# Optimization experiments

Hardware: AMD Instinct MI355X
Metric: run time of the kernel (lower is better)

The kernel has to match this reference:

```python
import jax, jax.numpy as jnp
import numpy as np

N = 100000      # nodes
E = 1200000     # edges (avg degree ~12)
D_IN = 64
D_OUT = 64


def setup_inputs() -> dict:
    key = jax.random.key(0)
    k1, k2, k3, k4 = jax.random.split(key, 4)
    x = jax.random.normal(k1, (N, D_IN), dtype=jnp.float32)
    # learned params (glorot-ish init)
    W = jax.random.normal(k2, (D_IN, D_OUT), dtype=jnp.float32) / np.sqrt(D_IN).astype(np.float32)
    b = jnp.zeros((D_OUT,), dtype=jnp.float32)
    src = jax.random.randint(k3, (E,), 0, N, dtype=jnp.int32)
    dst = jax.random.randint(k4, (E,), 0, N, dtype=jnp.int32)
    return {"x": x, "W": W, "b": b, "src": src, "dst": dst}


def reference(x, W, b, src, dst):
    # GCN layer: h = relu( D^-1/2 A D^-1/2 (x @ W) + b ), dropout=0 (eval)
    ones = jnp.ones(src.shape[0], dtype=x.dtype)
    deg_out = jax.ops.segment_sum(ones, src, num_segments=N)   # out-degree of source nodes
    deg_in = jax.ops.segment_sum(ones, dst, num_segments=N)    # in-degree of dest nodes
    norm_src = jax.lax.rsqrt(jnp.maximum(deg_out, 1.0))
    norm_dst = jax.lax.rsqrt(jnp.maximum(deg_in, 1.0))

    h = x @ W                                                  # [N, D_OUT] dense transform
    msg = h[src] * norm_src[src][:, None]                      # [E, D_OUT] gathered, pre-normalized messages
    agg = jax.ops.segment_sum(msg, dst, num_segments=N)        # [N, D_OUT] sparse aggregation
    out = agg * norm_dst[:, None] + b
    return jax.nn.relu(out)
```

## Files before the change

kernel.cpp:

```cpp
#include <hip/hip_runtime.h>
#include <hip/hip_bf16.h>

#define N_NODES 100000
#define N_EDGES 1200000
#define DCH 64

#define FB 256
#define NT 1024
#define EPB 4688
#define PPB 2344
#define HPAIRS 4688
#define GW_TOT (FB * NT / 64)

#define HALF_BINS 50000
#define HALF_WORDS 12500

#define BNODES 128
#define KBUK ((N_NODES + BNODES - 1) / BNODES)
#define CAPE 3008

#define NT2 512

#define OFF_DEG      0
#define OFF_GCUR     100096
#define OFF_FLAG     103296
#define OFF_ESORT    103424
#define OFF_HS       9512704

__device__ __forceinline__ float load_f(const void* p, int i, int f32) {
    if (f32) return ((const float*)p)[i];
    return __bfloat162float(((const __hip_bfloat16*)p)[i]);
}

__device__ __forceinline__ unsigned short f2bf_bits(float f) {
    __hip_bfloat16 h = __float2bfloat16(f);
    return __builtin_bit_cast(unsigned short, h);
}

__global__ __launch_bounds__(NT, 4)
void fused_kernel(const int* __restrict__ src,
                  const int* __restrict__ dst,
                  const void* __restrict__ x,
                  const void* __restrict__ W,
                  unsigned int* __restrict__ deg_packed,
                  int* __restrict__ gcur,
                  unsigned int* __restrict__ esort,
                  int* __restrict__ flag,
                  __hip_bfloat16* __restrict__ hs) {
    __shared__ unsigned int h[HALF_WORDS];
    int tid = threadIdx.x;
    int bid = blockIdx.x;

    int* sn = (int*)h;
    if (tid == 0) sn[0] = 0;
    __syncthreads();
    if (tid < 256) {
        const unsigned short* u = (const unsigned short*)x;
        int c = 0;
        for (int i = tid * 16; i < tid * 16 + 16; ++i) {
            unsigned short v = u[2 * i];
            int e = (v >> 7) & 0xFF;
            if (e >= 141) c++;
        }
        if (c) atomicAdd(sn, c);
    }
    __syncthreads();
    int f32 = sn[0] > 256;
    if (bid == 0 && tid == 0) *flag = f32;
    __syncthreads();

    {
        float* wt = (float*)h;
        for (int i = tid; i < DCH * DCH; i += NT) {
            int kk = i >> 6, cc = i & 63;
            wt[cc * 68 + kk] = load_f(W, i, f32);
        }
        __syncthreads();

        int lane = tid & 63;
        const float4* wrow = (const float4*)(wt + lane * 68);
        float wr[DCH];
#pragma unroll
        for (int kq = 0; kq < 16; ++kq) {
            float4 t = wrow[kq];
            wr[4 * kq + 0] = t.x; wr[4 * kq + 1] = t.y;
            wr[4 * kq + 2] = t.z; wr[4 * kq + 3] = t.w;
        }
#pragma unroll
        for (int kk = 0; kk < DCH; ++kk)
            asm volatile("" : "+v"(wr[kk]));

        int gw = (bid << 4) + (tid >> 6);
#define RLA(i) __int_as_float(__builtin_amdgcn_readlane(xiA, (i)))
#define RLB(i) __int_as_float(__builtin_amdgcn_readlane(xiB, (i)))
#define GRP(j) \
    a0 = fmaf(RLA(4*(j)+0), wr[4*(j)+0], a0); \
    a1 = fmaf(RLA(4*(j)+1), wr[4*(j)+1], a1); \
    a2 = fmaf(RLA(4*(j)+2), wr[4*(j)+2], a2); \
    a3 = fmaf(RLA(4*(j)+3), wr[4*(j)+3], a3); \
    c0 = fmaf(RLB(4*(j)+0), wr[4*(j)+0], c0); \
    c1 = fmaf(RLB(4*(j)+1), wr[4*(j)+1], c1); \
    c2 = fmaf(RLB(4*(j)+2), wr[4*(j)+2], c2); \
    c3 = fmaf(RLB(4*(j)+3), wr[4*(j)+3], c3);

        for (int node = gw; node < N_NODES; node += 2 * GW_TOT) {
            int nodeB = node + GW_TOT;
            int hasB = nodeB < N_NODES;
            float xvA = load_f(x, node * DCH + lane, f32);
            float xvB = hasB ? load_f(x, nodeB * DCH + lane, f32) : 0.0f;
            int xiA = __float_as_int(xvA);
            int xiB = __float_as_int(xvB);
            float a0 = 0.f, a1 = 0.f, a2 = 0.f, a3 = 0.f;
            float c0 = 0.f, c1 = 0.f, c2 = 0.f, c3 = 0.f;
            GRP(0)  GRP(1)  GRP(2)  GRP(3)
            GRP(4)  GRP(5)  GRP(6)  GRP(7)
            GRP(8)  GRP(9)  GRP(10) GRP(11)
            GRP(12) GRP(13) GRP(14) GRP(15)
            hs[node * DCH + lane] = __float2bfloat16((a0 + a1) + (a2 + a3));
            if (hasB)
                hs[nodeB * DCH + lane] = __float2bfloat16((c0 + c1) + (c2 + c3));
        }
#undef RLA
#undef RLB
#undef GRP
    }
    __syncthreads();

    {
        int half = bid & 1;
        int j = bid >> 1;
        int p0 = j * HPAIRS;
        int p1 = p0 + HPAIRS;
        if (p1 > N_EDGES / 2) p1 = N_EDGES / 2;
        const int2* s2 = (const int2*)src;
        for (int w = tid; w < HALF_WORDS; w += NT) h[w] = 0;
        __syncthreads();
        int lo = half * HALF_BINS;
        for (int p = p0 + tid; p < p1; p += NT) {
            int2 sp = s2[p];
            int n0 = sp.x - lo, n1 = sp.y - lo;
            if ((unsigned)n0 < (unsigned)HALF_BINS)
                atomicAdd(&h[n0 >> 2], 1u << ((n0 & 3) * 8));
            if ((unsigned)n1 < (unsigned)HALF_BINS)
                atomicAdd(&h[n1 >> 2], 1u << ((n1 & 3) * 8));
        }
        __syncthreads();
        unsigned int* dp = deg_packed + half * HALF_WORDS;
        for (int w = tid; w < HALF_WORDS; w += NT) {
            unsigned int v = h[w];
            if (v) atomicAdd(&dp[w], v);
        }
        __syncthreads();
    }

    {
        int e0 = bid * EPB;
        int eend = e0 + EPB; if (eend > N_EDGES) eend = N_EDGES;
        int npair = (eend - e0) >> 1;
        const int2* src2 = (const int2*)(src + e0);
        const int2* dst2 = (const int2*)(dst + e0);

        int* cnt  = (int*)h;
        int* base = cnt + KBUK;
        int* cur  = base + KBUK;
        for (int i = tid; i < KBUK; i += NT) { cnt[i] = 0; cur[i] = 0; }
        __syncthreads();
        for (int p = tid; p < npair; p += NT) {
            int2 dp = dst2[p];
            atomicAdd(&cnt[dp.x >> 7], 1);
            atomicAdd(&cnt[dp.y >> 7], 1);
        }
        __syncthreads();
        for (int i = tid; i < KBUK; i += NT)
            base[i] = atomicAdd(&gcur[i], cnt[i]);
        __syncthreads();
        for (int p = tid; p < npair; p += NT) {
            int2 sp = src2[p];
            int2 dp = dst2[p];
            int b0 = dp.x >> 7, b1 = dp.y >> 7;
            int pos0 = base[b0] + atomicAdd(&cur[b0], 1);
            if (pos0 < CAPE)
                esort[b0 * CAPE + pos0] =
                    (unsigned int)sp.x | ((unsigned int)(dp.x & 127) << 24);
            int pos1 = base[b1] + atomicAdd(&cur[b1], 1);
            if (pos1 < CAPE)
                esort[b1 * CAPE + pos1] =
                    (unsigned int)sp.y | ((unsigned int)(dp.y & 127) << 24);
        }
    }
}

__global__ __launch_bounds__(NT2, 6)
void sortgather_kernel(const __hip_bfloat16* __restrict__ hs,
                       const unsigned int* __restrict__ esort,
                       const int* __restrict__ gcur,
                       const unsigned int* __restrict__ deg_packed,
                       const void* __restrict__ b,
                       const int* __restrict__ flag,
                       void* __restrict__ out) {
    __shared__ unsigned int ebuf[CAPE];
    __shared__ int cnt[BNODES];
    __shared__ int loc[BNODES];
    __shared__ int sc[BNODES];
    __shared__ int cur[BNODES];
    __shared__ float tab[256];
    int k = blockIdx.x, tid = threadIdx.x;
    int bbase = k * CAPE;
    int m = gcur[k];
    if (m > CAPE) m = CAPE;

    if (tid < BNODES) { cnt[tid] = 0; cur[tid] = 0; }
    if (tid < 256) tab[tid] = rsqrtf(fmaxf((float)tid, 1.0f));
    __syncthreads();
    for (int e = tid; e < m; e += NT2)
        atomicAdd(&cnt[esort[bbase + e] >> 24], 1);
    __syncthreads();
    int v = 0;
    if (tid < BNODES) { v = cnt[tid]; sc[tid] = v; }
    __syncthreads();
    for (int off = 1; off < BNODES; off <<= 1) {
        int add = 0;
        if (tid < BNODES && tid >= off) add = sc[tid - off];
        __syncthreads();
        if (tid < BNODES) sc[tid] += add;
        __syncthreads();
    }
    if (tid < BNODES) loc[tid] = sc[tid] - v;
    __syncthreads();
    for (int e = tid; e < m; e += NT2) {
        unsigned int w = esort[bbase + e];
        int r = w >> 24;
        unsigned int s = w & 0xFFFFFFu;
        unsigned int dw = deg_packed[s >> 2];
        unsigned int degb = (dw >> ((s & 3) * 8)) & 0xFFu;
        int pos = loc[r] + atomicAdd(&cur[r], 1);
        ebuf[pos] = s | (degb << 24);
    }
    __syncthreads();

    int f32 = *flag;
    int lane = tid & 63, wv = tid >> 6;
    int q = lane >> 4;
    int cg = lane & 15;
    const unsigned short* hsu = (const unsigned short*)hs;
    float b0 = load_f(b, cg * 4 + 0, f32);
    float b1 = load_f(b, cg * 4 + 1, f32);
    float b2 = load_f(b, cg * 4 + 2, f32);
    float b3 = load_f(b, cg * 4 + 3, f32);
    int nlo = k * BNODES;

#define ACC(ACCV, U, F) \
    (ACCV).x = fmaf(__uint_as_float((U).x << 16),         (F), (ACCV).x); \
    (ACCV).y = fmaf(__uint_as_float((U).x & 0xFFFF0000u), (F), (ACCV).y); \
    (ACCV).z = fmaf(__uint_as_float((U).y << 16),         (F), (ACCV).z); \
    (ACCV).w = fmaf(__uint_as_float((U).y & 0xFFFF0000u), (F), (ACCV).w);

    for (int base = wv; base < BNODES; base += 16) {
        int tA = base, tB = base + 8;
        int nodeA = nlo + tA, nodeB = nlo + tB;
        int begA = loc[tA], degA = cnt[tA];
        int begB = loc[tB], degB = cnt[tB];
        float4 aA0 = {0.f,0.f,0.f,0.f}, aA1 = {0.f,0.f,0.f,0.f};
        float4 aA2 = {0.f,0.f,0.f,0.f}, aA3 = {0.f,0.f,0.f,0.f};
        float4 aB0 = {0.f,0.f,0.f,0.f}, aB1 = {0.f,0.f,0.f,0.f};
        float4 aB2 = {0.f,0.f,0.f,0.f}, aB3 = {0.f,0.f,0.f,0.f};
        int dmax = degA > degB ? degA : degB;
        for (int j0 = 0; j0 < dmax; j0 += 16) {
            int i0 = j0 + q, i1 = j0 + 4 + q, i2 = j0 + 8 + q, i3 = j0 + 12 + q;
            unsigned int wA0 = ebuf[(i0 < degA) ? (begA + i0) : 0];
            unsigned int wA1 = ebuf[(i1 < degA) ? (begA + i1) : 0];
            unsigned int wA2 = ebuf[(i2 < degA) ? (begA + i2) : 0];
            unsigned int wA3 = ebuf[(i3 < degA) ? (begA + i3) : 0];
            unsigned int wB0 = ebuf[(i0 < degB) ? (begB + i0) : 0];
            unsigned int wB1 = ebuf[(i1 < degB) ? (begB + i1) : 0];
            unsigned int wB2 = ebuf[(i2 < degB) ? (begB + i2) : 0];
            unsigned int wB3 = ebuf[(i3 < degB) ? (begB + i3) : 0];
            uint2 uA0 = ((const uint2*)(hsu + (wA0 & 0xFFFFFFu) * DCH))[cg];
            uint2 uA1 = ((const uint2*)(hsu + (wA1 & 0xFFFFFFu) * DCH))[cg];
            uint2 uA2 = ((const uint2*)(hsu + (wA2 & 0xFFFFFFu) * DCH))[cg];
            uint2 uA3 = ((const uint2*)(hsu + (wA3 & 0xFFFFFFu) * DCH))[cg];
            uint2 uB0 = ((const uint2*)(hsu + (wB0 & 0xFFFFFFu) * DCH))[cg];
            uint2 uB1 = ((const uint2*)(hsu + (wB1 & 0xFFFFFFu) * DCH))[cg];
            uint2 uB2 = ((const uint2*)(hsu + (wB2 & 0xFFFFFFu) * DCH))[cg];
            uint2 uB3 = ((const uint2*)(hsu + (wB3 & 0xFFFFFFu) * DCH))[cg];
            float fA0 = tab[wA0 >> 24], fA1 = tab[wA1 >> 24];
            float fA2 = tab[wA2 >> 24], fA3 = tab[wA3 >> 24];
            float fB0 = tab[wB0 >> 24], fB1 = tab[wB1 >> 24];
            float fB2 = tab[wB2 >> 24], fB3 = tab[wB3 >> 24];
            if (i0 < degA) { ACC(aA0, uA0, fA0) }
            if (i1 < degA) { ACC(aA1, uA1, fA1) }
            if (i2 < degA) { ACC(aA2, uA2, fA2) }
            if (i3 < degA) { ACC(aA3, uA3, fA3) }
            if (i0 < degB) { ACC(aB0, uB0, fB0) }
            if (i1 < degB) { ACC(aB1, uB1, fB1) }
            if (i2 < degB) { ACC(aB2, uB2, fB2) }
            if (i3 < degB) { ACC(aB3, uB3, fB3) }
        }
        float4 oA, oB;
        oA.x = (aA0.x + aA1.x) + (aA2.x + aA3.x);
        oA.y = (aA0.y + aA1.y) + (aA2.y + aA3.y);
        oA.z = (aA0.z + aA1.z) + (aA2.z + aA3.z);
        oA.w = (aA0.w + aA1.w) + (aA2.w + aA3.w);
        oB.x = (aB0.x + aB1.x) + (aB2.x + aB3.x);
        oB.y = (aB0.y + aB1.y) + (aB2.y + aB3.y);
        oB.z = (aB0.z + aB1.z) + (aB2.z + aB3.z);
        oB.w = (aB0.w + aB1.w) + (aB2.w + aB3.w);
        oA.x += __shfl_xor(oA.x, 16); oA.y += __shfl_xor(oA.y, 16);
        oA.z += __shfl_xor(oA.z, 16); oA.w += __shfl_xor(oA.w, 16);
        oA.x += __shfl_xor(oA.x, 32); oA.y += __shfl_xor(oA.y, 32);
        oA.z += __shfl_xor(oA.z, 32); oA.w += __shfl_xor(oA.w, 32);
        oB.x += __shfl_xor(oB.x, 16); oB.y += __shfl_xor(oB.y, 16);
        oB.z += __shfl_xor(oB.z, 16); oB.w += __shfl_xor(oB.w, 16);
        oB.x += __shfl_xor(oB.x, 32); oB.y += __shfl_xor(oB.y, 32);
        oB.z += __shfl_xor(oB.z, 32); oB.w += __shfl_xor(oB.w, 32);
        int myNode = (lane < 16) ? nodeA : nodeB;
        int myDeg  = (lane < 16) ? degA : degB;
        float4 o   = (lane < 16) ? oA : oB;
        if (lane < 32 && myNode < N_NODES) {
            float nrm = rsqrtf(fmaxf((float)myDeg, 1.0f));
            o.x = fmaxf(o.x * nrm + b0, 0.0f);
            o.y = fmaxf(o.y * nrm + b1, 0.0f);
            o.z = fmaxf(o.z * nrm + b2, 0.0f);
            o.w = fmaxf(o.w * nrm + b3, 0.0f);
            if (f32) {
                ((float4*)out)[myNode * 16 + cg] = o;
            } else {
                ushort4 s;
                s.x = f2bf_bits(o.x);
                s.y = f2bf_bits(o.y);
                s.z = f2bf_bits(o.z);
                s.w = f2bf_bits(o.w);
                ((ushort4*)out)[myNode * 16 + cg] = s;
            }
        }
    }
#undef ACC
}

extern "C" void kernel_launch(void* const* d_in, const int* in_sizes, int n_in,
                              void* d_out, int out_size, void* d_ws, size_t ws_size,
                              hipStream_t stream) {
    const void* x   = d_in[0];
    const void* W   = d_in[1];
    const void* b   = d_in[2];
    const int*  src = (const int*)d_in[3];
    const int*  dst = (const int*)d_in[4];

    char* ws = (char*)d_ws;
    unsigned int* deg_packed = (unsigned int*)(ws + OFF_DEG);
    int* gcur     = (int*)(ws + OFF_GCUR);
    int* flag     = (int*)(ws + OFF_FLAG);
    unsigned int* esort = (unsigned int*)(ws + OFF_ESORT);
    __hip_bfloat16* hs  = (__hip_bfloat16*)(ws + OFF_HS);

    (void)hipMemsetAsync(ws, 0, OFF_FLAG + 4, stream);

    fused_kernel<<<FB, NT, 0, stream>>>(
        src, dst, x, W, deg_packed, gcur, esort, flag, hs);

    sortgather_kernel<<<KBUK, NT2, 0, stream>>>(
        hs, esort, gcur, deg_packed, b, flag, d_out);
}
```

Baseline: 173.3 us.

## Replace bucketed sort with per-node edge lists and pre-normalized features

Restructures the pipeline into three kernels. The edge kernel builds per-node fixed-capacity adjacency lists (CAPN=48) using global atomics on a per-node counter, replacing the 128-node bucket sort plus in-block local sort. The GEMM kernel folds the source-degree normalization into the stored bf16 features, so the gather no longer needs a per-edge lookup of the norm factor. The gather kernel gives each wave two nodes and reads edge lists straight from global memory. The costs are heavy per-node global atomics with scattered writes, an extra launch, and silently dropped edges for any node with in-degree above 48.

```diff
diff --git a/kernel.cpp b/kernel.cpp
--- a/kernel.cpp
+++ b/kernel.cpp
@@ -3,29 +3,31 @@
 
 #define N_NODES 100000
 #define N_EDGES 1200000
+#define NPAIRS  (N_EDGES / 2)
 #define DCH 64
-
-#define FB 256
-#define NT 1024
-#define EPB 4688
-#define PPB 2344
-#define HPAIRS 4688
-#define GW_TOT (FB * NT / 64)
-
-#define HALF_BINS 50000
-#define HALF_WORDS 12500
-
-#define BNODES 128
-#define KBUK ((N_NODES + BNODES - 1) / BNODES)
-#define CAPE 3008
-
-#define NT2 512
+#define CAPN 48
+
+#define K1B 256
+#define K1T 1024
+#define NRID 8
+#define RID_NODES 12500
+#define RID_WORDS 3125
+#define SLICES (K1B / NRID)
+#define SLICE_PAIRS (NPAIRS / SLICES)
+#define SCAT_PAIRS ((NPAIRS + K1B - 1) / K1B)
+
+#define K2B 256
+#define K2T 1024
+#define GW_TOT (K2B * K2T / 64)
+
+#define K3T 512
+#define K3B (N_NODES / 16)
 
 #define OFF_DEG      0
 #define OFF_GCUR     100096
-#define OFF_FLAG     103296
-#define OFF_ESORT    103424
-#define OFF_HS       9512704
+#define OFF_FLAG     500096
+#define OFF_ESORT    500224
+#define OFF_HS       19700224
 
 __device__ __forceinline__ float load_f(const void* p, int i, int f32) {
     if (f32) return ((const float*)p)[i];
@@ -37,22 +39,85 @@
     return __builtin_bit_cast(unsigned short, h);
 }
 
-__global__ __launch_bounds__(NT, 4)
-void fused_kernel(const int* __restrict__ src,
+__global__ __launch_bounds__(K1T, 4)
+void edges_kernel(const int* __restrict__ src,
                   const int* __restrict__ dst,
                   const void* __restrict__ x,
-                  const void* __restrict__ W,
                   unsigned int* __restrict__ deg_packed,
                   int* __restrict__ gcur,
                   unsigned int* __restrict__ esort,
-                  int* __restrict__ flag,
-                  __hip_bfloat16* __restrict__ hs) {
-    __shared__ unsigned int h[HALF_WORDS];
-    int tid = threadIdx.x;
-    int bid = blockIdx.x;
-
-    int* sn = (int*)h;
-    if (tid == 0) sn[0] = 0;
+                  int* __restrict__ flag) {
+    __shared__ unsigned int h[RID_WORDS];
+    int tid = threadIdx.x, bid = blockIdx.x;
+
+    if (bid == 0) {
+        if (tid == 0) h[0] = 0;
+        __syncthreads();
+        if (tid < 256) {
+            const unsigned short* u = (const unsigned short*)x;
+            int c = 0;
+            for (int i = tid * 16; i < tid * 16 + 16; ++i) {
+                unsigned short v = u[2 * i];
+                int e = (v >> 7) & 0xFF;
+                if (e >= 141) c++;
+            }
+            if (c) atomicAdd(&h[0], (unsigned int)c);
+        }
+        __syncthreads();
+        if (tid == 0) *flag = (h[0] > 256) ? 1 : 0;
+        __syncthreads();
+    }
+
+    {
+        int rid = bid & (NRID - 1);
+        int j   = bid >> 3;
+        for (int w = tid; w < RID_WORDS; w += K1T) h[w] = 0;
+        __syncthreads();
+        int lo = rid * RID_NODES;
+        const int2* s2 = (const int2*)src;
+        int p0 = j * SLICE_PAIRS, p1 = p0 + SLICE_PAIRS;
+        for (int p = p0 + tid; p < p1; p += K1T) {
+            int2 sp = s2[p];
+            int n0 = sp.x - lo, n1 = sp.y - lo;
+            if ((unsigned)n0 < (unsigned)RID_NODES)
+                atomicAdd(&h[n0 >> 2], 1u << ((n0 & 3) * 8));
+            if ((unsigned)n1 < (unsigned)RID_NODES)
+                atomicAdd(&h[n1 >> 2], 1u << ((n1 & 3) * 8));
+        }
+        __syncthreads();
+        unsigned int* dp = deg_packed + rid * RID_WORDS;
+        for (int w = tid; w < RID_WORDS; w += K1T) {
+            unsigned int v = h[w];
+            if (v) atomicAdd(&dp[w], v);
+        }
+    }
+
+    {
+        int p0 = bid * SCAT_PAIRS;
+        int p1 = p0 + SCAT_PAIRS; if (p1 > NPAIRS) p1 = NPAIRS;
+        const int2* s2 = (const int2*)src;
+        const int2* d2 = (const int2*)dst;
+        for (int p = p0 + tid; p < p1; p += K1T) {
+            int2 sp = s2[p];
+            int2 dp = d2[p];
+            int pos0 = atomicAdd(&gcur[dp.x], 1);
+            if (pos0 < CAPN) esort[dp.x * CAPN + pos0] = (unsigned int)sp.x;
+            int pos1 = atomicAdd(&gcur[dp.y], 1);
+            if (pos1 < CAPN) esort[dp.y * CAPN + pos1] = (unsigned int)sp.y;
+        }
+    }
+}
+
+__global__ __launch_bounds__(K2T, 4)
+void gemm_kernel(const void* __restrict__ x,
+                 const void* __restrict__ W,
+                 const unsigned int* __restrict__ deg_packed,
+                 __hip_bfloat16* __restrict__ hs) {
+    __shared__ float wt[DCH * 68];
+    __shared__ int sn;
+    int tid = threadIdx.x, bid = blockIdx.x;
+
+    if (tid == 0) sn = 0;
     __syncthreads();
     if (tid < 256) {
         const unsigned short* u = (const unsigned short*)x;
@@ -62,35 +127,31 @@
             int e = (v >> 7) & 0xFF;
             if (e >= 141) c++;
         }
-        if (c) atomicAdd(sn, c);
+        if (c) atomicAdd(&sn, c);
     }
     __syncthreads();
-    int f32 = sn[0] > 256;
-    if (bid == 0 && tid == 0) *flag = f32;
+    int f32 = sn > 256;
+
+    for (int i = tid; i < DCH * DCH; i += K2T) {
+        int kk = i >> 6, cc = i & 63;
+        wt[cc * 68 + kk] = load_f(W, i, f32);
+    }
     __syncthreads();
 
-    {
-        float* wt = (float*)h;
-        for (int i = tid; i < DCH * DCH; i += NT) {
-            int kk = i >> 6, cc = i & 63;
-            wt[cc * 68 + kk] = load_f(W, i, f32);
-        }
-        __syncthreads();
-
-        int lane = tid & 63;
-        const float4* wrow = (const float4*)(wt + lane * 68);
-        float wr[DCH];
+    int lane = tid & 63;
+    const float4* wrow = (const float4*)(wt + lane * 68);
+    float wr[DCH];
 #pragma unroll
-        for (int kq = 0; kq < 16; ++kq) {
-            float4 t = wrow[kq];
-            wr[4 * kq + 0] = t.x; wr[4 * kq + 1] = t.y;
-            wr[4 * kq + 2] = t.z; wr[4 * kq + 3] = t.w;
-        }
+    for (int kq = 0; kq < 16; ++kq) {
+        float4 t = wrow[kq];
+        wr[4 * kq + 0] = t.x; wr[4 * kq + 1] = t.y;
+        wr[4 * kq + 2] = t.z; wr[4 * kq + 3] = t.w;
+    }
 #pragma unroll
-        for (int kk = 0; kk < DCH; ++kk)
-            asm volatile("" : "+v"(wr[kk]));
-
-        int gw = (bid << 4) + (tid >> 6);
+    for (int kk = 0; kk < DCH; ++kk)
+        asm volatile("" : "+v"(wr[kk]));
+
+    int gw = (bid << 4) + (tid >> 6);
 #define RLA(i) __int_as_float(__builtin_amdgcn_readlane(xiA, (i)))
 #define RLB(i) __int_as_float(__builtin_amdgcn_readlane(xiB, (i)))
 #define GRP(j) \
@@ -103,238 +164,140 @@
     c2 = fmaf(RLB(4*(j)+2), wr[4*(j)+2], c2); \
     c3 = fmaf(RLB(4*(j)+3), wr[4*(j)+3], c3);
 
-        for (int node = gw; node < N_NODES; node += 2 * GW_TOT) {
-            int nodeB = node + GW_TOT;
-            int hasB = nodeB < N_NODES;
-            float xvA = load_f(x, node * DCH + lane, f32);
-            float xvB = hasB ? load_f(x, nodeB * DCH + lane, f32) : 0.0f;
-            int xiA = __float_as_int(xvA);
-            int xiB = __float_as_int(xvB);
-            float a0 = 0.f, a1 = 0.f, a2 = 0.f, a3 = 0.f;
-            float c0 = 0.f, c1 = 0.f, c2 = 0.f, c3 = 0.f;
-            GRP(0)  GRP(1)  GRP(2)  GRP(3)
-            GRP(4)  GRP(5)  GRP(6)  GRP(7)
-            GRP(8)  GRP(9)  GRP(10) GRP(11)
-            GRP(12) GRP(13) GRP(14) GRP(15)
-            hs[node * DCH + lane] = __float2bfloat16((a0 + a1) + (a2 + a3));
-            if (hasB)
-                hs[nodeB * DCH + lane] = __float2bfloat16((c0 + c1) + (c2 + c3));
-        }
+    for (int node = gw; node < N_NODES; node += 2 * GW_TOT) {
+        int nodeB = node + GW_TOT;
+        int hasB = nodeB < N_NODES;
+        float xvA = load_f(x, node * DCH + lane, f32);
+        float xvB = hasB ? load_f(x, nodeB * DCH + lane, f32) : 0.0f;
+        int xiA = __float_as_int(xvA);
+        int xiB = __float_as_int(xvB);
+        float a0 = 0.f, a1 = 0.f, a2 = 0.f, a3 = 0.f;
+        float c0 = 0.f, c1 = 0.f, c2 = 0.f, c3 = 0.f;
+        GRP(0)  GRP(1)  GRP(2)  GRP(3)
+        GRP(4)  GRP(5)  GRP(6)  GRP(7)
+        GRP(8)  GRP(9)  GRP(10) GRP(11)
+        GRP(12) GRP(13) GRP(14) GRP(15)
+        unsigned int dwA = deg_packed[node >> 2];
+        float dgA = (float)((dwA >> ((node & 3) * 8)) & 0xFFu);
+        float nrA = rsqrtf(fmaxf(dgA, 1.0f));
+        hs[node * DCH + lane] = __float2bfloat16(((a0 + a1) + (a2 + a3)) * nrA);
+        if (hasB) {
+            unsigned int dwB = deg_packed[nodeB >> 2];
+            float dgB = (float)((dwB >> ((nodeB & 3) * 8)) & 0xFFu);
+            float nrB = rsqrtf(fmaxf(dgB, 1.0f));
+            hs[nodeB * DCH + lane] = __float2bfloat16(((c0 + c1) + (c2 + c3)) * nrB);
+        }
+    }
 #undef RLA
 #undef RLB
 #undef GRP
-    }
-    __syncthreads();
-
-    {
-        int half = bid & 1;
-        int j = bid >> 1;
-        int p0 = j * HPAIRS;
-        int p1 = p0 + HPAIRS;
-        if (p1 > N_EDGES / 2) p1 = N_EDGES / 2;
-        const int2* s2 = (const int2*)src;
-        for (int w = tid; w < HALF_WORDS; w += NT) h[w] = 0;
-        __syncthreads();
-        int lo = half * HALF_BINS;
-        for (int p = p0 + tid; p < p1; p += NT) {
-            int2 sp = s2[p];
-            int n0 = sp.x - lo, n1 = sp.y - lo;
-            if ((unsigned)n0 < (unsigned)HALF_BINS)
-                atomicAdd(&h[n0 >> 2], 1u << ((n0 & 3) * 8));
-            if ((unsigned)n1 < (unsigned)HALF_BINS)
-                atomicAdd(&h[n1 >> 2], 1u << ((n1 & 3) * 8));
-        }
-        __syncthreads();
-        unsigned int* dp = deg_packed + half * HALF_WORDS;
-        for (int w = tid; w < HALF_WORDS; w += NT) {
-            unsigned int v = h[w];
-            if (v) atomicAdd(&dp[w], v);
-        }
-        __syncthreads();
-    }
-
-    {
-        int e0 = bid * EPB;
-        int eend = e0 + EPB; if (eend > N_EDGES) eend = N_EDGES;
-        int npair = (eend - e0) >> 1;
-        const int2* src2 = (const int2*)(src + e0);
-        const int2* dst2 = (const int2*)(dst + e0);
-
-        int* cnt  = (int*)h;
-        int* base = cnt + KBUK;
-        int* cur  = base + KBUK;
-        for (int i = tid; i < KBUK; i += NT) { cnt[i] = 0; cur[i] = 0; }
-        __syncthreads();
-        for (int p = tid; p < npair; p += NT) {
-            int2 dp = dst2[p];
-            atomicAdd(&cnt[dp.x >> 7], 1);
-            atomicAdd(&cnt[dp.y >> 7], 1);
-        }
-        __syncthreads();
-        for (int i = tid; i < KBUK; i += NT)
-            base[i] = atomicAdd(&gcur[i], cnt[i]);
-        __syncthreads();
-        for (int p = tid; p < npair; p += NT) {
-            int2 sp = src2[p];
-            int2 dp = dst2[p];
-            int b0 = dp.x >> 7, b1 = dp.y >> 7;
-            int pos0 = base[b0] + atomicAdd(&cur[b0], 1);
-            if (pos0 < CAPE)
-                esort[b0 * CAPE + pos0] =
-                    (unsigned int)sp.x | ((unsigned int)(dp.x & 127) << 24);
-            int pos1 = base[b1] + atomicAdd(&cur[b1], 1);
-            if (pos1 < CAPE)
-                esort[b1 * CAPE + pos1] =
-                    (unsigned int)sp.y | ((unsigned int)(dp.y & 127) << 24);
-        }
-    }
-}
-
-__global__ __launch_bounds__(NT2, 6)
-void sortgather_kernel(const __hip_bfloat16* __restrict__ hs,
-                       const unsigned int* __restrict__ esort,
-                       const int* __restrict__ gcur,
-                       const unsigned int* __restrict__ deg_packed,
-                       const void* __restrict__ b,
-                       const int* __restrict__ flag,
-                       void* __restrict__ out) {
-    __shared__ unsigned int ebuf[CAPE];
-    __shared__ int cnt[BNODES];
-    __shared__ int loc[BNODES];
-    __shared__ int sc[BNODES];
-    __shared__ int cur[BNODES];
-    __shared__ float tab[256];
-    int k = blockIdx.x, tid = threadIdx.x;
-    int bbase = k * CAPE;
-    int m = gcur[k];
-    if (m > CAPE) m = CAPE;
-
-    if (tid < BNODES) { cnt[tid] = 0; cur[tid] = 0; }
-    if (tid < 256) tab[tid] = rsqrtf(fmaxf((float)tid, 1.0f));
-    __syncthreads();
-    for (int e = tid; e < m; e += NT2)
-        atomicAdd(&cnt[esort[bbase + e] >> 24], 1);
-    __syncthreads();
-    int v = 0;
-    if (tid < BNODES) { v = cnt[tid]; sc[tid] = v; }
-    __syncthreads();
-    for (int off = 1; off < BNODES; off <<= 1) {
-        int add = 0;
-        if (tid < BNODES && tid >= off) add = sc[tid - off];
-        __syncthreads();
-        if (tid < BNODES) sc[tid] += add;
-        __syncthreads();
-    }
-    if (tid < BNODES) loc[tid] = sc[tid] - v;
-    __syncthreads();
-    for (int e = tid; e < m; e += NT2) {
-        unsigned int w = esort[bbase + e];
-        int r = w >> 24;
-        unsigned int s = w & 0xFFFFFFu;
-        unsigned int dw = deg_packed[s >> 2];
-        unsigned int degb = (dw >> ((s & 3) * 8)) & 0xFFu;
-        int pos = loc[r] + atomicAdd(&cur[r], 1);
-        ebuf[pos] = s | (degb << 24);
-    }
-    __syncthreads();
-
-    int f32 = *flag;
-    int lane = tid & 63, wv = tid >> 6;
+}
+
+__global__ __launch_bounds__(K3T, 4)
+void gather_kernel(const __hip_bfloat16* __restrict__ hs,
+                   const unsigned int* __restrict__ esort,
+                   const int* __restrict__ gcur,
+                   const void* __restrict__ b,
+                   const int* __restrict__ flag,
+                   void* __restrict__ out) {
+    int tid = threadIdx.x;
+    int lane = tid & 63;
+    int wave = blockIdx.x * (K3T / 64) + (tid >> 6);
     int q = lane >> 4;
     int cg = lane & 15;
-    const unsigned short* hsu = (const unsigned short*)hs;
+    int f32 = *flag;
     float b0 = load_f(b, cg * 4 + 0, f32);
     float b1 = load_f(b, cg * 4 + 1, f32);
     float b2 = load_f(b, cg * 4 + 2, f32);
     float b3 = load_f(b, cg * 4 + 3, f32);
-    int nlo = k * BNODES;
-
-#define ACC(ACCV, U, F) \
-    (ACCV).x = fmaf(__uint_as_float((U).x << 16),         (F), (ACCV).x); \
-    (ACCV).y = fmaf(__uint_as_float((U).x & 0xFFFF0000u), (F), (ACCV).y); \
-    (ACCV).z = fmaf(__uint_as_float((U).y << 16),         (F), (ACCV).z); \
-    (ACCV).w = fmaf(__uint_as_float((U).y & 0xFFFF0000u), (F), (ACCV).w);
-
-    for (int base = wv; base < BNODES; base += 16) {
-        int tA = base, tB = base + 8;
-        int nodeA = nlo + tA, nodeB = nlo + tB;
-        int begA = loc[tA], degA = cnt[tA];
-        int begB = loc[tB], degB = cnt[tB];
-        float4 aA0 = {0.f,0.f,0.f,0.f}, aA1 = {0.f,0.f,0.f,0.f};
-        float4 aA2 = {0.f,0.f,0.f,0.f}, aA3 = {0.f,0.f,0.f,0.f};
-        float4 aB0 = {0.f,0.f,0.f,0.f}, aB1 = {0.f,0.f,0.f,0.f};
-        float4 aB2 = {0.f,0.f,0.f,0.f}, aB3 = {0.f,0.f,0.f,0.f};
-        int dmax = degA > degB ? degA : degB;
-        for (int j0 = 0; j0 < dmax; j0 += 16) {
-            int i0 = j0 + q, i1 = j0 + 4 + q, i2 = j0 + 8 + q, i3 = j0 + 12 + q;
-            unsigned int wA0 = ebuf[(i0 < degA) ? (begA + i0) : 0];
-            unsigned int wA1 = ebuf[(i1 < degA) ? (begA + i1) : 0];
-            unsigned int wA2 = ebuf[(i2 < degA) ? (begA + i2) : 0];
-            unsigned int wA3 = ebuf[(i3 < degA) ? (begA + i3) : 0];
-            unsigned int wB0 = ebuf[(i0 < degB) ? (begB + i0) : 0];
-            unsigned int wB1 = ebuf[(i1 < degB) ? (begB + i1) : 0];
-            unsigned int wB2 = ebuf[(i2 < degB) ? (begB + i2) : 0];
-            unsigned int wB3 = ebuf[(i3 < degB) ? (begB + i3) : 0];
-            uint2 uA0 = ((const uint2*)(hsu + (wA0 & 0xFFFFFFu) * DCH))[cg];
-            uint2 uA1 = ((const uint2*)(hsu + (wA1 & 0xFFFFFFu) * DCH))[cg];
-            uint2 uA2 = ((const uint2*)(hsu + (wA2 & 0xFFFFFFu) * DCH))[cg];
-            uint2 uA3 = ((const uint2*)(hsu + (wA3 & 0xFFFFFFu) * DCH))[cg];
-            uint2 uB0 = ((const uint2*)(hsu + (wB0 & 0xFFFFFFu) * DCH))[cg];
-            uint2 uB1 = ((const uint2*)(hsu + (wB1 & 0xFFFFFFu) * DCH))[cg];
-            uint2 uB2 = ((const uint2*)(hsu + (wB2 & 0xFFFFFFu) * DCH))[cg];
-            uint2 uB3 = ((const uint2*)(hsu + (wB3 & 0xFFFFFFu) * DCH))[cg];
-            float fA0 = tab[wA0 >> 24], fA1 = tab[wA1 >> 24];
-            float fA2 = tab[wA2 >> 24], fA3 = tab[wA3 >> 24];
-            float fB0 = tab[wB0 >> 24], fB1 = tab[wB1 >> 24];
-            float fB2 = tab[wB2 >> 24], fB3 = tab[wB3 >> 24];
-            if (i0 < degA) { ACC(aA0, uA0, fA0) }
-            if (i1 < degA) { ACC(aA1, uA1, fA1) }
-            if (i2 < degA) { ACC(aA2, uA2, fA2) }
-            if (i3 < degA) { ACC(aA3, uA3, fA3) }
-            if (i0 < degB) { ACC(aB0, uB0, fB0) }
-            if (i1 < degB) { ACC(aB1, uB1, fB1) }
-            if (i2 < degB) { ACC(aB2, uB2, fB2) }
-            if (i3 < degB) { ACC(aB3, uB3, fB3) }
-        }
-        float4 oA, oB;
-        oA.x = (aA0.x + aA1.x) + (aA2.x + aA3.x);
-        oA.y = (aA0.y + aA1.y) + (aA2.y + aA3.y);
-        oA.z = (aA0.z + aA1.z) + (aA2.z + aA3.z);
-        oA.w = (aA0.w + aA1.w) + (aA2.w + aA3.w);
-        oB.x = (aB0.x + aB1.x) + (aB2.x + aB3.x);
-        oB.y = (aB0.y + aB1.y) + (aB2.y + aB3.y);
-        oB.z = (aB0.z + aB1.z) + (aB2.z + aB3.z);
-        oB.w = (aB0.w + aB1.w) + (aB2.w + aB3.w);
-        oA.x += __shfl_xor(oA.x, 16); oA.y += __shfl_xor(oA.y, 16);
-        oA.z += __shfl_xor(oA.z, 16); oA.w += __shfl_xor(oA.w, 16);
-        oA.x += __shfl_xor(oA.x, 32); oA.y += __shfl_xor(oA.y, 32);
-        oA.z += __shfl_xor(oA.z, 32); oA.w += __shfl_xor(oA.w, 32);
-        oB.x += __shfl_xor(oB.x, 16); oB.y += __shfl_xor(oB.y, 16);
-        oB.z += __shfl_xor(oB.z, 16); oB.w += __shfl_xor(oB.w, 16);
-        oB.x += __shfl_xor(oB.x, 32); oB.y += __shfl_xor(oB.y, 32);
-        oB.z += __shfl_xor(oB.z, 32); oB.w += __shfl_xor(oB.w, 32);
-        int myNode = (lane < 16) ? nodeA : nodeB;
-        int myDeg  = (lane < 16) ? degA : degB;
-        float4 o   = (lane < 16) ? oA : oB;
-        if (lane < 32 && myNode < N_NODES) {
-            float nrm = rsqrtf(fmaxf((float)myDeg, 1.0f));
-            o.x = fmaxf(o.x * nrm + b0, 0.0f);
-            o.y = fmaxf(o.y * nrm + b1, 0.0f);
-            o.z = fmaxf(o.z * nrm + b2, 0.0f);
-            o.w = fmaxf(o.w * nrm + b3, 0.0f);
-            if (f32) {
-                ((float4*)out)[myNode * 16 + cg] = o;
-            } else {
-                ushort4 s;
-                s.x = f2bf_bits(o.x);
-                s.y = f2bf_bits(o.y);
-                s.z = f2bf_bits(o.z);
-                s.w = f2bf_bits(o.w);
-                ((ushort4*)out)[myNode * 16 + cg] = s;
-            }
-        }
+
+    int nodeA = wave * 2, nodeB = nodeA + 1;
+    int degAt = gcur[nodeA], degBt = gcur[nodeB];
+    int dA = degAt < CAPN ? degAt : CAPN;
+    int dB = degBt < CAPN ? degBt : CAPN;
+    const unsigned int* eA = esort + nodeA * CAPN;
+    const unsigned int* eB = esort + nodeB * CAPN;
+    const unsigned short* hsu = (const unsigned short*)hs;
+
+    float4 aA0 = {0.f,0.f,0.f,0.f}, aA1 = {0.f,0.f,0.f,0.f};
+    float4 aA2 = {0.f,0.f,0.f,0.f}, aA3 = {0.f,0.f,0.f,0.f};
+    float4 aB0 = {0.f,0.f,0.f,0.f}, aB1 = {0.f,0.f,0.f,0.f};
+    float4 aB2 = {0.f,0.f,0.f,0.f}, aB3 = {0.f,0.f,0.f,0.f};
+
+#define ACC(ACCV, U) \
+    (ACCV).x += __uint_as_float((U).x << 16); \
+    (ACCV).y += __uint_as_float((U).x & 0xFFFF0000u); \
+    (ACCV).z += __uint_as_float((U).y << 16); \
+    (ACCV).w += __uint_as_float((U).y & 0xFFFF0000u);
+
+    int dmax = dA > dB ? dA : dB;
+    for (int j0 = 0; j0 < dmax; j0 += 16) {
+        int i0 = j0 + q, i1 = j0 + 4 + q, i2 = j0 + 8 + q, i3 = j0 + 12 + q;
+        unsigned int sA0 = (i0 < dA) ? eA[i0] : 0u;
+        unsigned int sA1 = (i1 < dA) ? eA[i1] : 0u;
+        unsigned int sA2 = (i2 < dA) ? eA[i2] : 0u;
+        unsigned int sA3 = (i3 < dA) ? eA[i3] : 0u;
+        unsigned int sB0 = (i0 < dB) ? eB[i0] : 0u;
+        unsigned int sB1 = (i1 < dB) ? eB[i1] : 0u;
+        unsigned int sB2 = (i2 < dB) ? eB[i2] : 0u;
+        unsigned int sB3 = (i3 < dB) ? eB[i3] : 0u;
+        uint2 uA0 = ((const uint2*)(hsu + sA0 * DCH))[cg];
+        uint2 uA1 = ((const uint2*)(hsu + sA1 * DCH))[cg];
+        uint2 uA2 = ((const uint2*)(hsu + sA2 * DCH))[cg];
+        uint2 uA3 = ((const uint2*)(hsu + sA3 * DCH))[cg];
+        uint2 uB0 = ((const uint2*)(hsu + sB0 * DCH))[cg];
+        uint2 uB1 = ((const uint2*)(hsu + sB1 * DCH))[cg];
+        uint2 uB2 = ((const uint2*)(hsu + sB2 * DCH))[cg];
+        uint2 uB3 = ((const uint2*)(hsu + sB3 * DCH))[cg];
+        if (i0 < dA) { ACC(aA0, uA0) }
+        if (i1 < dA) { ACC(aA1, uA1) }
+        if (i2 < dA) { ACC(aA2, uA2) }
+        if (i3 < dA) { ACC(aA3, uA3) }
+        if (i0 < dB) { ACC(aB0, uB0) }
+        if (i1 < dB) { ACC(aB1, uB1) }
+        if (i2 < dB) { ACC(aB2, uB2) }
+        if (i3 < dB) { ACC(aB3, uB3) }
     }
 #undef ACC
+
+    float4 oA, oB;
+    oA.x = (aA0.x + aA1.x) + (aA2.x + aA3.x);
+    oA.y = (aA0.y + aA1.y) + (aA2.y + aA3.y);
+    oA.z = (aA0.z + aA1.z) + (aA2.z + aA3.z);
+    oA.w = (aA0.w + aA1.w) + (aA2.w + aA3.w);
+    oB.x = (aB0.x + aB1.x) + (aB2.x + aB3.x);
+    oB.y = (aB0.y + aB1.y) + (aB2.y + aB3.y);
+    oB.z = (aB0.z + aB1.z) + (aB2.z + aB3.z);
+    oB.w = (aB0.w + aB1.w) + (aB2.w + aB3.w);
+    oA.x += __shfl_xor(oA.x, 16); oA.y += __shfl_xor(oA.y, 16);
+    oA.z += __shfl_xor(oA.z, 16); oA.w += __shfl_xor(oA.w, 16);
+    oA.x += __shfl_xor(oA.x, 32); oA.y += __shfl_xor(oA.y, 32);
+    oA.z += __shfl_xor(oA.z, 32); oA.w += __shfl_xor(oA.w, 32);
+    oB.x += __shfl_xor(oB.x, 16); oB.y += __shfl_xor(oB.y, 16);
+    oB.z += __shfl_xor(oB.z, 16); oB.w += __shfl_xor(oB.w, 16);
+    oB.x += __shfl_xor(oB.x, 32); oB.y += __shfl_xor(oB.y, 32);
+    oB.z += __shfl_xor(oB.z, 32); oB.w += __shfl_xor(oB.w, 32);
+
+    int myNode = (lane < 16) ? nodeA : nodeB;
+    int myDeg  = (lane < 16) ? degAt : degBt;
+    float4 o   = (lane < 16) ? oA : oB;
+    if (lane < 32) {
+        float nrm = rsqrtf(fmaxf((float)myDeg, 1.0f));
+        o.x = fmaxf(o.x * nrm + b0, 0.0f);
+        o.y = fmaxf(o.y * nrm + b1, 0.0f);
+        o.z = fmaxf(o.z * nrm + b2, 0.0f);
+        o.w = fmaxf(o.w * nrm + b3, 0.0f);
+        if (f32) {
+            ((float4*)out)[myNode * 16 + cg] = o;
+        } else {
+            ushort4 s;
+            s.x = f2bf_bits(o.x);
+            s.y = f2bf_bits(o.y);
+            s.z = f2bf_bits(o.z);
+            s.w = f2bf_bits(o.w);
+            ((ushort4*)out)[myNode * 16 + cg] = s;
+        }
+    }
 }
 
 extern "C" void kernel_launch(void* const* d_in, const int* in_sizes, int n_in,
@@ -355,9 +318,10 @@
 
     (void)hipMemsetAsync(ws, 0, OFF_FLAG + 4, stream);
 
-    fused_kernel<<<FB, NT, 0, stream>>>(
-        src, dst, x, W, deg_packed, gcur, esort, flag, hs);
-
-    sortgather_kernel<<<KBUK, NT2, 0, stream>>>(
-        hs, esort, gcur, deg_packed, b, flag, d_out);
-}
+    edges_kernel<<<K1B, K1T, 0, stream>>>(
+        src, dst, x, deg_packed, gcur, esort, flag);
+
+    gemm_kernel<<<K2B, K2T, 0, stream>>>(x, W, deg_packed, hs);
+
+    gather_kernel<<<K3B, K3T, 0, stream>>>(hs, esort, gcur, b, flag, d_out);
+}
```

After: 268.9 us. +55.2%, slower.
